# Kernel optimization log

Measured on AMD Instinct MI355X. Metric: run time of the kernel, lower is better.

Reference implementation:

```python
import jax, jax.numpy as jnp
import numpy as np
from jax import lax

EPS = 1e-4  # BatchNorm eps from the module

def maxpool2x2(x):
    # x: [N, C, H, W] -> 2x2 max pool, stride 2, no padding
    return lax.reduce_window(x, -jnp.inf, lax.max, (1, 1, 2, 2), (1, 1, 2, 2), 'VALID')

def conv_nchw(x, w):
    return lax.conv_general_dilated(x, w, window_strides=(1, 1), padding='VALID',
                                    dimension_numbers=('NCHW', 'OIHW', 'NCHW'))

def setup_inputs() -> dict:
    key = jax.random.key(0)
    ks = jax.random.split(key, 6)
    return {
        'x':       jax.random.normal(ks[0], (8192, 1, 32, 32), dtype=jnp.float32),
        'conv1_w': jax.random.normal(ks[1], (20, 1, 5, 5), dtype=jnp.float32) * 0.1,
        'conv2_w': jax.random.normal(ks[2], (50, 20, 5, 5), dtype=jnp.float32) * 0.1,
        'lin_w':   jax.random.normal(ks[3], (500, 1250), dtype=jnp.float32) * 0.05,
        'fc_w':    jax.random.normal(ks[4], (10, 500), dtype=jnp.float32) * 0.05,
        'fc_b':    jax.random.normal(ks[5], (10,), dtype=jnp.float32) * 0.05,
    }

def reference(x, conv1_w, conv2_w, lin_w, fc_w, fc_b):
    # --- features ---
    # Conv2d(1, 20, k=5, bias=False): [N,1,32,32] -> [N,20,28,28]
    h = conv_nchw(x, conv1_w)
    # BatchNorm2d(20, eps=1e-4, affine=False), training-mode batch stats (biased var)
    mean = jnp.mean(h, axis=(0, 2, 3), keepdims=True)
    var = jnp.var(h, axis=(0, 2, 3), keepdims=True)
    h = (h - mean) * lax.rsqrt(var + EPS)
    # ReLU + MaxPool 2x2: -> [N,20,14,14]
    h = maxpool2x2(jnp.maximum(h, 0.0))
    # Binarize(): sign of activations
    h = jnp.sign(h)
    # Conv2dBinary(20, 50, k=5): XNOR-style conv = conv with sign(W), scaled by
    # per-output-channel alpha = mean(|W|). -> [N,50,10,10]
    alpha2 = jnp.mean(jnp.abs(conv2_w), axis=(1, 2, 3)).reshape(1, -1, 1, 1)
    h = conv_nchw(h, jnp.sign(conv2_w)) * alpha2
    # Hardtanh + MaxPool 2x2: -> [N,50,5,5]
    h = maxpool2x2(jnp.clip(h, -1.0, 1.0))
    # --- dense ---
    h = h.reshape(h.shape[0], -1)  # [N, 1250], channel-major like torch.flatten
    h = jnp.sign(h)
    # LinearBinary(1250, 500): y = x @ sign(W)^T * alpha, alpha = mean(|W|, dim=1)
    alpha_l = jnp.mean(jnp.abs(lin_w), axis=1)  # [500]
    h = (h @ jnp.sign(lin_w).T) * alpha_l
    h = jnp.clip(h, -1.0, 1.0)
    # fc: Linear(500, num_classes)
    return h @ fc_w.T + fc_b
```

## Files before the change

### kernel.cpp

```cpp
#include <hip/hip_runtime.h>
#include <stdint.h>


#define NIMG 8192

typedef __attribute__((ext_vector_type(8))) _Float16 f16x8;
typedef __attribute__((ext_vector_type(16))) float f32x16;
typedef __attribute__((ext_vector_type(4))) int i32x4;
typedef __attribute__((ext_vector_type(16))) int i32x16;


__global__ __launch_bounds__(256) void prepsum_k(const float* __restrict__ lw,
                                                 const float* __restrict__ w2,
                                                 const float* __restrict__ x,
                                                 unsigned long long* __restrict__ lwp,
                                                 float* __restrict__ alpha,
                                                 i32x4* __restrict__ bg,
                                                 float* __restrict__ partial) {
  int b = blockIdx.x, tid = threadIdx.x;
  if (b < 125) {
    int wave = tid >> 6, lane = tid & 63;
    int j = b * 4 + wave;
    float pa = 0.f;
    for (int k = lane; k < 1250; k += 64) pa += fabsf(lw[j * 1250 + k]);
    for (int o = 32; o > 0; o >>= 1) pa += __shfl_down(pa, o, 64);
    if (lane == 0) alpha[j] = pa / 1250.0f;
    if (lane < 20) {
      unsigned long long m = 0;
      int base = j * 1250 + lane * 64;
      int lim = 1250 - lane * 64; if (lim > 64) lim = 64;
      for (int bb = 0; bb < lim; ++bb)
        if (lw[base + bb] > 0.f) m |= (1ull << bb);
      lwp[j * 20 + lane] = m;
    }
  } else if (b < 138) {
    int idx = (b - 125) * 256 + tid;
    if (idx < 3200) {
      int t = idx >> 7;
      int rem = idx & 127;
      int l = rem & 63;
      int nt = rem >> 6;
      int oc = nt * 32 + (l & 31);
      int hi = l >> 5;
      i32x4 o4;
#pragma unroll
      for (int wi = 0; wi < 4; ++wi) {
        int word = 0;
#pragma unroll
        for (int bb = 0; bb < 4; ++bb) {
          int k = hi * 16 + wi * 4 + bb;
          int v = 0;
          if (k < 20 && oc < 50)
            v = (w2[(oc * 20 + k) * 25 + t] > 0.f) ? 1 : -1;
          word |= (v & 0xff) << (8 * bb);
        }
        o4[wi] = word;
      }
      bg[idx] = o4;
    }
  } else {
    int sb = b - 138;
    const float4* xv = (const float4*)x + (size_t)sb * 16 * 256;
    float ax = 0.f, ay = 0.f, az = 0.f, aw = 0.f;
    for (int nn = 0; nn < 16; ++nn) {
      float4 v = xv[nn * 256 + tid];
      ax += v.x; ay += v.y; az += v.z; aw += v.w;
    }
    float4 r; r.x = ax; r.y = ay; r.z = az; r.w = aw;
    ((float4*)(partial + (size_t)sb * 1024))[tid] = r;
  }
}

__global__ __launch_bounds__(256) void reduce_k(const float* __restrict__ partial,
                                                float* __restrict__ partial2) {
  int b = blockIdx.x, tid = threadIdx.x;
  int e = (b & 3) * 256 + tid;
  int p0 = (b >> 2) * 32;
  float s = 0.f;
#pragma unroll
  for (int p = 0; p < 32; ++p) s += partial[(size_t)(p0 + p) * 1024 + e];
  partial2[(size_t)(b >> 2) * 1024 + e] = s;
}

__global__ __launch_bounds__(256) void mean_k(const float* __restrict__ partial2,
                                              const float* __restrict__ w1,
                                              float* __restrict__ mean) {
  __shared__ float Tsh[1024];
  __shared__ double U8[25][8];
  __shared__ double U[25];
  int t = threadIdx.x;
  for (int e = t; e < 1024; e += 256) {
    double s = 0.0;
#pragma unroll
    for (int b = 0; b < 16; ++b) s += (double)partial2[b * 1024 + e];
    Tsh[e] = (float)s;
  }
  __syncthreads();
  if (t < 200) {
    int tap = t >> 3, part = t & 7;
    int ky = tap / 5, kx = tap % 5;
    double s = 0.0;
    for (int p = part * 98; p < part * 98 + 98; ++p) {
      int py = p / 28, px = p % 28;
      s += (double)Tsh[(py + ky) * 32 + px + kx];
    }
    U8[tap][part] = s;
  }
  __syncthreads();
  if (t < 25) {
    double s = 0.0;
    for (int i = 0; i < 8; ++i) s += U8[t][i];
    U[t] = s;
  }
  __syncthreads();
  if (t < 20) {
    double s = 0.0;
    for (int q = 0; q < 25; ++q) s += (double)w1[t * 25 + q] * U[q];
    mean[t] = (float)(s / (8192.0 * 784.0));
  }
}

__device__ inline uint32_t pack_f16_pair(float fv) {
  _Float16 h = (_Float16)fv;
  float rem = fv - (float)h;
  _Float16 l = (_Float16)(rem * 4096.0f);
  uint32_t hb = (uint32_t)__builtin_bit_cast(unsigned short, h);
  uint32_t lb = (uint32_t)__builtin_bit_cast(unsigned short, l);
  return (hb << 16) | lb;
}

__global__ __launch_bounds__(256, 6) void conv1_mfma_k(const float* __restrict__ x,
                                                       const float* __restrict__ w1,
                                                       const float* __restrict__ mean,
                                                       uint32_t* __restrict__ b1p) {
  __shared__ uint32_t xs[1032];
  int tid = threadIdx.x;
  int wave = tid >> 6, lane = tid & 63;
  int n = blockIdx.x;

  const float4* xin = (const float4*)(x + (size_t)n * 1024);
  {
    float4 v = xin[tid];
    float fv[4] = {v.x, v.y, v.z, v.w};
#pragma unroll
    for (int e = 0; e < 4; ++e)
      xs[4 * tid + e] = pack_f16_pair(fv[e]);
  }
  if (tid < 8) xs[1024 + tid] = 0;

  int bc = lane & 31;
  int khsel = lane >> 5;
  f16x8 Bh[2], Bhs[2], Bl[2];
  const int t1tab[8] = {8, 9, 18, 19, 20, 21, 22, 23};
  const _Float16 SC = (_Float16)4096.0f;
#pragma unroll
  for (int j = 0; j < 8; ++j) {
    int t0 = j + khsel * 10;
    float wv0 = (bc < 20) ? w1[bc * 25 + t0] : 0.f;
    uint32_t p0 = pack_f16_pair(wv0);
    _Float16 h0 = __builtin_bit_cast(_Float16, (unsigned short)(p0 >> 16));
    Bh[0][j] = h0;
    Bhs[0][j] = h0 * SC;
    Bl[0][j] = __builtin_bit_cast(_Float16, (unsigned short)(p0 & 0xffffu));
    float wv1 = 0.f;
    if (bc < 20) {
      if (khsel == 0) wv1 = w1[bc * 25 + t1tab[j]];
      else if (j == 4) wv1 = w1[bc * 25 + 24];
    }
    uint32_t p1 = pack_f16_pair(wv1);
    _Float16 h1 = __builtin_bit_cast(_Float16, (unsigned short)(p1 >> 16));
    Bh[1][j] = h1;
    Bhs[1][j] = h1 * SC;
    Bl[1][j] = __builtin_bit_cast(_Float16, (unsigned short)(p1 & 0xffffu));
  }
  float mv = (bc < 20) ? mean[bc] * 4096.0f : 3.0e38f;

  int m = lane & 31;
  int d0 = m + khsel * 64;
  int d1 = m + khsel * 4;

  __syncthreads();

  int pp0 = (wave < 2) ? wave * 4 : 8 + (wave - 2) * 3;
  int cnt = (wave < 2) ? 4 : 3;
  for (int pp = pp0; pp < pp0 + cnt; ++pp) {
    unsigned long long bacc[16];
#pragma unroll
    for (int r = 0; r < 16; ++r) bacc[r] = 0ull;
#pragma unroll
    for (int py2 = 0; py2 < 2; ++py2) {
      int pybase = (2 * pp + py2) * 32;
      const uint32_t* b0 = xs + pybase + d0;
      const uint32_t* b1 = xs + pybase + d1;
      uint32_t raw[16];
      raw[0] = b0[0];   raw[1] = b0[1];   raw[2] = b0[2];   raw[3] = b0[3];
      raw[4] = b0[4];   raw[5] = b0[32];  raw[6] = b0[33];  raw[7] = b0[34];
      raw[8] = b1[35];  raw[9] = b1[36];  raw[10] = b1[99]; raw[11] = b1[100];
      raw[12] = b1[128]; raw[13] = b1[129]; raw[14] = b1[130]; raw[15] = b1[131];
      f16x8 Ah[2], Al[2];
#pragma unroll
      for (int kh = 0; kh < 2; ++kh) {
        uint32_t hw[4], lw2[4];
#pragma unroll
        for (int jj = 0; jj < 4; ++jj) {
          uint32_t v0 = raw[kh * 8 + 2 * jj], v1 = raw[kh * 8 + 2 * jj + 1];
          hw[jj] = __builtin_amdgcn_perm(v1, v0, 0x07060302u);
          lw2[jj] = __builtin_amdgcn_perm(v1, v0, 0x05040100u);
        }
        struct U4 { uint32_t a, b, c, d; };
        U4 hv4 = {hw[0], hw[1], hw[2], hw[3]};
        U4 lv4 = {lw2[0], lw2[1], lw2[2], lw2[3]};
        Ah[kh] = __builtin_bit_cast(f16x8, hv4);
        Al[kh] = __builtin_bit_cast(f16x8, lv4);
      }
      f32x16 acc;
#pragma unroll
      for (int i = 0; i < 16; ++i) acc[i] = 0.f;
      acc = __builtin_amdgcn_mfma_f32_32x32x16_f16(Ah[0], Bhs[0], acc, 0, 0, 0);
      acc = __builtin_amdgcn_mfma_f32_32x32x16_f16(Ah[1], Bhs[1], acc, 0, 0, 0);
      acc = __builtin_amdgcn_mfma_f32_32x32x16_f16(Ah[0], Bl[0], acc, 0, 0, 0);
      acc = __builtin_amdgcn_mfma_f32_32x32x16_f16(Ah[1], Bl[1], acc, 0, 0, 0);
      acc = __builtin_amdgcn_mfma_f32_32x32x16_f16(Al[0], Bh[0], acc, 0, 0, 0);
      acc = __builtin_amdgcn_mfma_f32_32x32x16_f16(Al[1], Bh[1], acc, 0, 0, 0);
#pragma unroll
      for (int r = 0; r < 16; ++r)
        bacc[r] |= __ballot(acc[r] > mv);
    }
    uint32_t pm = 0;
#pragma unroll
    for (int pc = 0; pc < 14; ++pc) {
      int px0 = 2 * pc;
      int r0 = (px0 & 3) + 4 * (px0 >> 3);
      int h0 = (px0 >> 2) & 1;
      unsigned long long mm = bacc[r0] | bacc[r0 + 1];
      uint32_t val = (uint32_t)(mm >> (32 * h0));
      if (lane == pc) pm = val;
    }
    if (lane < 14) b1p[(size_t)n * 196 + pp * 14 + lane] = pm;
  }
}

__global__ __launch_bounds__(512, 6) void conv2lin_k(const uint32_t* __restrict__ b1p,
                                                     const i32x4* __restrict__ bg,
                                                     const unsigned long long* __restrict__ lwp,
                                                     const float* __restrict__ alpha,
                                                     const float* __restrict__ fcw,
                                                     const float* __restrict__ fcb,
                                                     float* __restrict__ out) {
  __shared__ uint32_t b1sh[1568];
  __shared__ __attribute__((aligned(16))) char uni[8][2048];
  int tid = threadIdx.x;
  int wave = tid >> 6, lane = tid & 63;
  int n0 = blockIdx.x * 8;

#pragma unroll
  for (int r = 0; r < 4; ++r) {
    int idx = r * 512 + tid;
    if (idx < 1568) b1sh[idx] = b1p[(size_t)n0 * 196 + idx];
  }
  __syncthreads();

  {
    int m = lane & 31, hi = lane >> 5;
    int shbase = hi * 16;
    for (int mt = wave; mt < 25; mt += 8) {
      int qg = mt * 8 + (m >> 2);
      int img = (qg * 41) >> 10;
      int quad = qg - img * 25;
      int Y = (quad * 13) >> 6;
      int X = quad - Y * 5;
      int px = (2 * Y + ((m >> 1) & 1)) * 14 + 2 * X + (m & 1);
      const uint32_t* arow = b1sh + img * 196 + px;
      const i32x4* bgl = bg + lane;
      i32x16 acc0, acc1;
#pragma unroll
      for (int i = 0; i < 16; ++i) { acc0[i] = 0; acc1[i] = 0; }
#pragma unroll 1
      for (int ky = 0; ky < 5; ++ky) {
        const uint32_t* ar2 = arow + ky * 14;
        const i32x4* bg2 = bgl + ky * 5 * 128;
#pragma unroll
        for (int kx = 0; kx < 5; ++kx) {
          uint32_t w = ar2[kx];
          i32x4 av;
#pragma unroll
          for (int wi = 0; wi < 4; ++wi)
            av[wi] = (int)((((w >> (shbase + 4 * wi)) & 0xFu) * 0x00204081u) & 0x01010101u);
          i32x4 bv0 = bg2[kx * 128];
          i32x4 bv1 = bg2[kx * 128 + 64];
          acc0 = __builtin_amdgcn_mfma_i32_32x32x32_i8(av, bv0, acc0, 0, 0, 0);
          acc1 = __builtin_amdgcn_mfma_i32_32x32x32_i8(av, bv1, acc1, 0, 0, 0);
        }
      }
      int oc0 = m, oc1 = 32 + m;
#pragma unroll
      for (int g = 0; g < 4; ++g) {
        int qloc = 2 * g + hi;
        int qg2 = mt * 8 + qloc;
        int img2 = (qg2 * 41) >> 10;
        int quad2 = qg2 - img2 * 25;
        {
          int a0 = acc0[4 * g], a1 = acc0[4 * g + 1], a2 = acc0[4 * g + 2], a3 = acc0[4 * g + 3];
          int c0 = a0 > a1 ? a0 : a1, c1 = a2 > a3 ? a2 : a3;
          int best = c0 > c1 ? c0 : c1;
          uni[img2][oc0 * 25 + quad2] = (char)((best > 0) - (best < 0));
        }
        if (oc1 < 50) {
          int a0 = acc1[4 * g], a1 = acc1[4 * g + 1], a2 = acc1[4 * g + 2], a3 = acc1[4 * g + 3];
          int c0 = a0 > a1 ? a0 : a1, c1 = a2 > a3 ? a2 : a3;
          int best = c0 > c1 ? c0 : c1;
          uni[img2][oc1 * 25 + quad2] = (char)((best > 0) - (best < 0));
        }
      }
    }
  }
  __syncthreads();

  int n = n0 + wave;
  signed char* s2w = (signed char*)uni[wave];
  float* hshw = (float*)uni[wave];
  if (lane < 30) s2w[1250 + lane] = 0;

  unsigned long long Pm[20], Nm[20];
  int cp = 0, cn = 0;
#pragma unroll
  for (int k = 0; k < 20; ++k) {
    signed char v = s2w[k * 64 + lane];
    unsigned long long P = __ballot(v > 0);
    unsigned long long N = __ballot(v < 0);
    Pm[k] = P; Nm[k] = N;
    cp += __popcll(P); cn += __popcll(N);
  }

#pragma unroll
  for (int rd = 0; rd < 8; ++rd) {
    int j = rd * 64 + lane;
    float y = 0.f;
    if (j < 500) {
      const ulonglong2* W2 = (const ulonglong2*)(lwp + (size_t)j * 20);
      int a = 0, b = 0;
#pragma unroll
      for (int i = 0; i < 10; ++i) {
        ulonglong2 w2v = W2[i];
        a += __popcll(w2v.x & Pm[2 * i]) + __popcll(w2v.y & Pm[2 * i + 1]);
        b += __popcll(w2v.x & Nm[2 * i]) + __popcll(w2v.y & Nm[2 * i + 1]);
      }
      int dot = 2 * (a - b) - cp + cn;
      y = alpha[j] * (float)dot;
      y = fminf(1.0f, fmaxf(-1.0f, y));
    }
    hshw[rd * 64 + lane] = y;
  }

  float hv[8];
#pragma unroll
  for (int k = 0; k < 8; ++k) hv[k] = hshw[k * 64 + lane];
#pragma unroll
  for (int o = 0; o < 10; ++o) {
    float pa = 0.f;
#pragma unroll
    for (int k = 0; k < 8; ++k) {
      int j = k * 64 + lane;
      if (j < 500) pa += hv[k] * fcw[o * 500 + j];
    }
    for (int off = 32; off > 0; off >>= 1) pa += __shfl_down(pa, off, 64);
    if (lane == 0) out[(size_t)n * 10 + o] = pa + fcb[o];
  }
}

extern "C" void kernel_launch(void* const* d_in, const int* in_sizes, int n_in,
                              void* d_out, int out_size, void* d_ws, size_t ws_size,
                              hipStream_t stream) {
  const float* x   = (const float*)d_in[0];
  const float* w1  = (const float*)d_in[1];
  const float* w2  = (const float*)d_in[2];
  const float* lw  = (const float*)d_in[3];
  const float* fcw = (const float*)d_in[4];
  const float* fcb = (const float*)d_in[5];
  float* out = (float*)d_out;
  char* ws = (char*)d_ws;

  float*    mean  = (float*)(ws + 0);
  float*    alpha = (float*)(ws + 5632);
  unsigned long long* lwp = (unsigned long long*)(ws + 7680);
  float*    partial = (float*)(ws + 87808);
  uint32_t* b1p   = (uint32_t*)(ws + 2184960);
  float*    partial2 = (float*)(ws + 8607488);
  i32x4*    bg    = (i32x4*)(ws + 8673024);

  prepsum_k<<<650, 256, 0, stream>>>(lw, w2, x, lwp, alpha, bg, partial);
  reduce_k<<<64, 256, 0, stream>>>(partial, partial2);
  mean_k<<<1, 256, 0, stream>>>(partial2, w1, mean);
  conv1_mfma_k<<<8192, 256, 0, stream>>>(x, w1, mean, b1p);
  conv2lin_k<<<1024, 512, 0, stream>>>(b1p, bg, lwp, alpha, fcw, fcb, out);
}
```

Baseline: 230.6 us.

## Fuse conv1 MFMA stage into conv2/linear kernel, keep pooled bits in LDS

Merges the per-image conv1 kernel into the conv2+linear kernel. Each of the 8 waves now computes conv1, BN threshold and pooling for its own image into shared memory, with no global b1p round trip. This removes one kernel launch and the global write and read of the packed conv1 bitmaps. In exchange LDS use grows by about 33KB per block, occupancy is capped at 4 blocks, and each wave runs all 14 pooled rows serially instead of splitting them across 4 waves.

```diff
diff --git a/kernel.cpp b/kernel.cpp
--- a/kernel.cpp
+++ b/kernel.cpp
@@ -129,134 +129,125 @@
   return (hb << 16) | lb;
 }
 
-__global__ __launch_bounds__(256, 6) void conv1_mfma_k(const float* __restrict__ x,
-                                                       const float* __restrict__ w1,
-                                                       const float* __restrict__ mean,
-                                                       uint32_t* __restrict__ b1p) {
-  __shared__ uint32_t xs[1032];
-  int tid = threadIdx.x;
-  int wave = tid >> 6, lane = tid & 63;
-  int n = blockIdx.x;
-
-  const float4* xin = (const float4*)(x + (size_t)n * 1024);
-  {
-    float4 v = xin[tid];
-    float fv[4] = {v.x, v.y, v.z, v.w};
-#pragma unroll
-    for (int e = 0; e < 4; ++e)
-      xs[4 * tid + e] = pack_f16_pair(fv[e]);
-  }
-  if (tid < 8) xs[1024 + tid] = 0;
-
-  int bc = lane & 31;
-  int khsel = lane >> 5;
-  f16x8 Bh[2], Bhs[2], Bl[2];
-  const int t1tab[8] = {8, 9, 18, 19, 20, 21, 22, 23};
-  const _Float16 SC = (_Float16)4096.0f;
-#pragma unroll
-  for (int j = 0; j < 8; ++j) {
-    int t0 = j + khsel * 10;
-    float wv0 = (bc < 20) ? w1[bc * 25 + t0] : 0.f;
-    uint32_t p0 = pack_f16_pair(wv0);
-    _Float16 h0 = __builtin_bit_cast(_Float16, (unsigned short)(p0 >> 16));
-    Bh[0][j] = h0;
-    Bhs[0][j] = h0 * SC;
-    Bl[0][j] = __builtin_bit_cast(_Float16, (unsigned short)(p0 & 0xffffu));
-    float wv1 = 0.f;
-    if (bc < 20) {
-      if (khsel == 0) wv1 = w1[bc * 25 + t1tab[j]];
-      else if (j == 4) wv1 = w1[bc * 25 + 24];
-    }
-    uint32_t p1 = pack_f16_pair(wv1);
-    _Float16 h1 = __builtin_bit_cast(_Float16, (unsigned short)(p1 >> 16));
-    Bh[1][j] = h1;
-    Bhs[1][j] = h1 * SC;
-    Bl[1][j] = __builtin_bit_cast(_Float16, (unsigned short)(p1 & 0xffffu));
-  }
-  float mv = (bc < 20) ? mean[bc] * 4096.0f : 3.0e38f;
-
-  int m = lane & 31;
-  int d0 = m + khsel * 64;
-  int d1 = m + khsel * 4;
-
-  __syncthreads();
-
-  int pp0 = (wave < 2) ? wave * 4 : 8 + (wave - 2) * 3;
-  int cnt = (wave < 2) ? 4 : 3;
-  for (int pp = pp0; pp < pp0 + cnt; ++pp) {
-    unsigned long long bacc[16];
-#pragma unroll
-    for (int r = 0; r < 16; ++r) bacc[r] = 0ull;
-#pragma unroll
-    for (int py2 = 0; py2 < 2; ++py2) {
-      int pybase = (2 * pp + py2) * 32;
-      const uint32_t* b0 = xs + pybase + d0;
-      const uint32_t* b1 = xs + pybase + d1;
-      uint32_t raw[16];
-      raw[0] = b0[0];   raw[1] = b0[1];   raw[2] = b0[2];   raw[3] = b0[3];
-      raw[4] = b0[4];   raw[5] = b0[32];  raw[6] = b0[33];  raw[7] = b0[34];
-      raw[8] = b1[35];  raw[9] = b1[36];  raw[10] = b1[99]; raw[11] = b1[100];
-      raw[12] = b1[128]; raw[13] = b1[129]; raw[14] = b1[130]; raw[15] = b1[131];
-      f16x8 Ah[2], Al[2];
-#pragma unroll
-      for (int kh = 0; kh < 2; ++kh) {
-        uint32_t hw[4], lw2[4];
-#pragma unroll
-        for (int jj = 0; jj < 4; ++jj) {
-          uint32_t v0 = raw[kh * 8 + 2 * jj], v1 = raw[kh * 8 + 2 * jj + 1];
-          hw[jj] = __builtin_amdgcn_perm(v1, v0, 0x07060302u);
-          lw2[jj] = __builtin_amdgcn_perm(v1, v0, 0x05040100u);
-        }
-        struct U4 { uint32_t a, b, c, d; };
-        U4 hv4 = {hw[0], hw[1], hw[2], hw[3]};
-        U4 lv4 = {lw2[0], lw2[1], lw2[2], lw2[3]};
-        Ah[kh] = __builtin_bit_cast(f16x8, hv4);
-        Al[kh] = __builtin_bit_cast(f16x8, lv4);
-      }
-      f32x16 acc;
-#pragma unroll
-      for (int i = 0; i < 16; ++i) acc[i] = 0.f;
-      acc = __builtin_amdgcn_mfma_f32_32x32x16_f16(Ah[0], Bhs[0], acc, 0, 0, 0);
-      acc = __builtin_amdgcn_mfma_f32_32x32x16_f16(Ah[1], Bhs[1], acc, 0, 0, 0);
-      acc = __builtin_amdgcn_mfma_f32_32x32x16_f16(Ah[0], Bl[0], acc, 0, 0, 0);
-      acc = __builtin_amdgcn_mfma_f32_32x32x16_f16(Ah[1], Bl[1], acc, 0, 0, 0);
-      acc = __builtin_amdgcn_mfma_f32_32x32x16_f16(Al[0], Bh[0], acc, 0, 0, 0);
-      acc = __builtin_amdgcn_mfma_f32_32x32x16_f16(Al[1], Bh[1], acc, 0, 0, 0);
-#pragma unroll
-      for (int r = 0; r < 16; ++r)
-        bacc[r] |= __ballot(acc[r] > mv);
-    }
-    uint32_t pm = 0;
-#pragma unroll
-    for (int pc = 0; pc < 14; ++pc) {
-      int px0 = 2 * pc;
-      int r0 = (px0 & 3) + 4 * (px0 >> 3);
-      int h0 = (px0 >> 2) & 1;
-      unsigned long long mm = bacc[r0] | bacc[r0 + 1];
-      uint32_t val = (uint32_t)(mm >> (32 * h0));
-      if (lane == pc) pm = val;
-    }
-    if (lane < 14) b1p[(size_t)n * 196 + pp * 14 + lane] = pm;
-  }
-}
-
-__global__ __launch_bounds__(512, 6) void conv2lin_k(const uint32_t* __restrict__ b1p,
-                                                     const i32x4* __restrict__ bg,
-                                                     const unsigned long long* __restrict__ lwp,
-                                                     const float* __restrict__ alpha,
-                                                     const float* __restrict__ fcw,
-                                                     const float* __restrict__ fcb,
-                                                     float* __restrict__ out) {
+__global__ __launch_bounds__(512, 4) void conv12_k(const float* __restrict__ x,
+                                                   const float* __restrict__ w1,
+                                                   const float* __restrict__ mean,
+                                                   const i32x4* __restrict__ bg,
+                                                   const unsigned long long* __restrict__ lwp,
+                                                   const float* __restrict__ alpha,
+                                                   const float* __restrict__ fcw,
+                                                   const float* __restrict__ fcb,
+                                                   float* __restrict__ out) {
+  __shared__ uint32_t xs8[8][1032];
   __shared__ uint32_t b1sh[1568];
   __shared__ __attribute__((aligned(16))) char uni[8][2048];
   int tid = threadIdx.x;
   int wave = tid >> 6, lane = tid & 63;
   int n0 = blockIdx.x * 8;
-
-#pragma unroll
-  for (int r = 0; r < 4; ++r) {
-    int idx = r * 512 + tid;
-    if (idx < 1568) b1sh[idx] = b1p[(size_t)n0 * 196 + idx];
+  int n = n0 + wave;
+
+  uint32_t* xs = xs8[wave];
+  {
+    const float4* xin = (const float4*)(x + (size_t)n * 1024);
+#pragma unroll
+    for (int i = 0; i < 4; ++i) {
+      int idx = i * 64 + lane;
+      float4 v = xin[idx];
+      float fv[4] = {v.x, v.y, v.z, v.w};
+#pragma unroll
+      for (int e = 0; e < 4; ++e)
+        xs[4 * idx + e] = pack_f16_pair(fv[e]);
+    }
+    if (lane < 8) xs[1024 + lane] = 0;
+  }
+
+  int bc = lane & 31;
+  int khsel = lane >> 5;
+  {
+    f16x8 Bh[2], Bhs[2], Bl[2];
+    const int t1tab[8] = {8, 9, 18, 19, 20, 21, 22, 23};
+    const _Float16 SC = (_Float16)4096.0f;
+#pragma unroll
+    for (int j = 0; j < 8; ++j) {
+      int t0 = j + khsel * 10;
+      float wv0 = (bc < 20) ? w1[bc * 25 + t0] : 0.f;
+      uint32_t p0 = pack_f16_pair(wv0);
+      _Float16 h0 = __builtin_bit_cast(_Float16, (unsigned short)(p0 >> 16));
+      Bh[0][j] = h0;
+      Bhs[0][j] = h0 * SC;
+      Bl[0][j] = __builtin_bit_cast(_Float16, (unsigned short)(p0 & 0xffffu));
+      float wv1 = 0.f;
+      if (bc < 20) {
+        if (khsel == 0) wv1 = w1[bc * 25 + t1tab[j]];
+        else if (j == 4) wv1 = w1[bc * 25 + 24];
+      }
+      uint32_t p1 = pack_f16_pair(wv1);
+      _Float16 h1 = __builtin_bit_cast(_Float16, (unsigned short)(p1 >> 16));
+      Bh[1][j] = h1;
+      Bhs[1][j] = h1 * SC;
+      Bl[1][j] = __builtin_bit_cast(_Float16, (unsigned short)(p1 & 0xffffu));
+    }
+    float mv = (bc < 20) ? mean[bc] * 4096.0f : 3.0e38f;
+
+    int m = lane & 31;
+    int d0 = m + khsel * 64;
+    int d1 = m + khsel * 4;
+
+    for (int pp = 0; pp < 14; ++pp) {
+      unsigned long long bacc[16];
+#pragma unroll
+      for (int r = 0; r < 16; ++r) bacc[r] = 0ull;
+#pragma unroll
+      for (int py2 = 0; py2 < 2; ++py2) {
+        int pybase = (2 * pp + py2) * 32;
+        const uint32_t* b0 = xs + pybase + d0;
+        const uint32_t* b1 = xs + pybase + d1;
+        uint32_t raw[16];
+        raw[0] = b0[0];   raw[1] = b0[1];   raw[2] = b0[2];   raw[3] = b0[3];
+        raw[4] = b0[4];   raw[5] = b0[32];  raw[6] = b0[33];  raw[7] = b0[34];
+        raw[8] = b1[35];  raw[9] = b1[36];  raw[10] = b1[99]; raw[11] = b1[100];
+        raw[12] = b1[128]; raw[13] = b1[129]; raw[14] = b1[130]; raw[15] = b1[131];
+        f16x8 Ah[2], Al[2];
+#pragma unroll
+        for (int kh = 0; kh < 2; ++kh) {
+          uint32_t hw[4], lw2[4];
+#pragma unroll
+          for (int jj = 0; jj < 4; ++jj) {
+            uint32_t v0 = raw[kh * 8 + 2 * jj], v1 = raw[kh * 8 + 2 * jj + 1];
+            hw[jj] = __builtin_amdgcn_perm(v1, v0, 0x07060302u);
+            lw2[jj] = __builtin_amdgcn_perm(v1, v0, 0x05040100u);
+          }
+          struct U4 { uint32_t a, b, c, d; };
+          U4 hv4 = {hw[0], hw[1], hw[2], hw[3]};
+          U4 lv4 = {lw2[0], lw2[1], lw2[2], lw2[3]};
+          Ah[kh] = __builtin_bit_cast(f16x8, hv4);
+          Al[kh] = __builtin_bit_cast(f16x8, lv4);
+        }
+        f32x16 acc;
+#pragma unroll
+        for (int i = 0; i < 16; ++i) acc[i] = 0.f;
+        acc = __builtin_amdgcn_mfma_f32_32x32x16_f16(Ah[0], Bhs[0], acc, 0, 0, 0);
+        acc = __builtin_amdgcn_mfma_f32_32x32x16_f16(Ah[1], Bhs[1], acc, 0, 0, 0);
+        acc = __builtin_amdgcn_mfma_f32_32x32x16_f16(Ah[0], Bl[0], acc, 0, 0, 0);
+        acc = __builtin_amdgcn_mfma_f32_32x32x16_f16(Ah[1], Bl[1], acc, 0, 0, 0);
+        acc = __builtin_amdgcn_mfma_f32_32x32x16_f16(Al[0], Bh[0], acc, 0, 0, 0);
+        acc = __builtin_amdgcn_mfma_f32_32x32x16_f16(Al[1], Bh[1], acc, 0, 0, 0);
+#pragma unroll
+        for (int r = 0; r < 16; ++r)
+          bacc[r] |= __ballot(acc[r] > mv);
+      }
+      uint32_t pm = 0;
+#pragma unroll
+      for (int pc = 0; pc < 14; ++pc) {
+        int px0 = 2 * pc;
+        int r0 = (px0 & 3) + 4 * (px0 >> 3);
+        int h0 = (px0 >> 2) & 1;
+        unsigned long long mm = bacc[r0] | bacc[r0 + 1];
+        uint32_t val = (uint32_t)(mm >> (32 * h0));
+        if (lane == pc) pm = val;
+      }
+      if (lane < 14) b1sh[wave * 196 + pp * 14 + lane] = pm;
+    }
   }
   __syncthreads();
 
@@ -316,7 +307,6 @@
   }
   __syncthreads();
 
-  int n = n0 + wave;
   signed char* s2w = (signed char*)uni[wave];
   float* hshw = (float*)uni[wave];
   if (lane < 30) s2w[1250 + lane] = 0;
@@ -384,13 +374,11 @@
   float*    alpha = (float*)(ws + 5632);
   unsigned long long* lwp = (unsigned long long*)(ws + 7680);
   float*    partial = (float*)(ws + 87808);
-  uint32_t* b1p   = (uint32_t*)(ws + 2184960);
   float*    partial2 = (float*)(ws + 8607488);
   i32x4*    bg    = (i32x4*)(ws + 8673024);
 
   prepsum_k<<<650, 256, 0, stream>>>(lw, w2, x, lwp, alpha, bg, partial);
   reduce_k<<<64, 256, 0, stream>>>(partial, partial2);
   mean_k<<<1, 256, 0, stream>>>(partial2, w1, mean);
-  conv1_mfma_k<<<8192, 256, 0, stream>>>(x, w1, mean, b1p);
-  conv2lin_k<<<1024, 512, 0, stream>>>(b1p, bg, lwp, alpha, fcw, fcb, out);
-}
+  conv12_k<<<1024, 512, 0, stream>>>(x, w1, mean, bg, lwp, alpha, fcw, fcb, out);
+}
```

New measurement: 219.4 us. -4.8%, faster.
